# Kernel optimization log

Measured on AMD Instinct MI355X. Metric: run time of the kernel, lower is better.

The kernel has to match this reference:

```python
import jax, jax.numpy as jnp
import numpy as np

B, N, D, H = 4, 2048, 256, 4
HD = D // H


def _linear(x, W, b):
    return x @ W.T + b


def _rotate_half(x):
    # pairs (x0,x1) -> (-x1, x0)
    x1 = x[..., ::2]
    x2 = x[..., 1::2]
    return jnp.stack((-x2, x1), axis=-1).reshape(x.shape)


def _layernorm(x, g, b, eps=1e-5):
    m = jnp.mean(x, axis=-1, keepdims=True)
    v = jnp.mean((x - m) ** 2, axis=-1, keepdims=True)
    return (x - m) / jnp.sqrt(v + eps) * g + b


def _ffn(x, W1, b1, g, be, W2, b2):
    h = _linear(x, W1, b1)
    h = _layernorm(h, g, be)
    h = jax.nn.gelu(h, approximate=False)
    return _linear(h, W2, b2)


def _self_block(x, enc, Wqkv, bqkv, Wout, bout, W1, b1, g, be, W2, b2):
    Bq, Nq, _ = x.shape
    qkv = _linear(x, Wqkv, bqkv).reshape(Bq, Nq, H, HD, 3).transpose(0, 2, 1, 3, 4)  # [B,H,N,HD,3]
    q, k, v = qkv[..., 0], qkv[..., 1], qkv[..., 2]
    q = q * enc[0] + _rotate_half(q) * enc[1]
    k = k * enc[0] + _rotate_half(k) * enc[1]
    scale = HD ** -0.5
    sim = jnp.einsum('bhid,bhjd->bhij', q, k) * scale
    attn = jax.nn.softmax(sim, axis=-1)
    ctx = jnp.einsum('bhij,bhjd->bhid', attn, v)
    msg = _linear(ctx.transpose(0, 2, 1, 3).reshape(Bq, Nq, D), Wout, bout)
    return x + _ffn(jnp.concatenate([x, msg], axis=-1), W1, b1, g, be, W2, b2)


def _cross_block(x0, x1, Wqk, bqk, Wv, bv, Wo, bo, W1, b1, g, be, W2, b2):
    def heads(t):
        return t.reshape(t.shape[0], t.shape[1], H, HD).transpose(0, 2, 1, 3)  # [B,H,N,HD]
    qk0 = heads(_linear(x0, Wqk, bqk))
    qk1 = heads(_linear(x1, Wqk, bqk))
    v0 = heads(_linear(x0, Wv, bv))
    v1 = heads(_linear(x1, Wv, bv))
    s = (HD ** -0.5) ** 0.5
    qk0 = qk0 * s
    qk1 = qk1 * s
    sim = jnp.einsum('bhid,bhjd->bhij', qk0, qk1)
    attn01 = jax.nn.softmax(sim, axis=-1)   # over j (x1 tokens)
    attn10 = jax.nn.softmax(sim, axis=-2)   # over i (x0 tokens)
    m0 = jnp.einsum('bhij,bhjd->bhid', attn01, v1)
    m1 = jnp.einsum('bhij,bhid->bhjd', attn10, v0)
    def unheads(t):
        return t.transpose(0, 2, 1, 3).reshape(t.shape[0], t.shape[2], D)
    m0 = _linear(unheads(m0), Wo, bo)
    m1 = _linear(unheads(m1), Wo, bo)
    x0 = x0 + _ffn(jnp.concatenate([x0, m0], axis=-1), W1, b1, g, be, W2, b2)
    x1 = x1 + _ffn(jnp.concatenate([x1, m1], axis=-1), W1, b1, g, be, W2, b2)
    return x0, x1


def setup_inputs() -> dict:
    key = jax.random.key(0)
    ks = jax.random.split(key, 32)
    std = 0.05

    def rn(k, shape, s=std):
        return jax.random.normal(k, shape, dtype=jnp.float32) * s

    def enc(k):
        ang = jax.random.uniform(k, (B, 1, N, HD // 2), dtype=jnp.float32) * (2 * np.pi)
        cos = jnp.repeat(jnp.cos(ang), 2, axis=-1)
        sin = jnp.repeat(jnp.sin(ang), 2, axis=-1)
        return jnp.stack([cos, sin], axis=0)  # [2,B,1,N,HD]

    return {
        'desc0': rn(ks[0], (B, N, D), 1.0),
        'desc1': rn(ks[1], (B, N, D), 1.0),
        'enc0': enc(ks[2]),
        'enc1': enc(ks[3]),
        's_Wqkv': rn(ks[4], (3 * D, D)), 's_bqkv': jnp.zeros((3 * D,), jnp.float32),
        's_Wout': rn(ks[5], (D, D)), 's_bout': jnp.zeros((D,), jnp.float32),
        's_W1': rn(ks[6], (2 * D, 2 * D)), 's_b1': jnp.zeros((2 * D,), jnp.float32),
        's_g': jnp.ones((2 * D,), jnp.float32), 's_be': jnp.zeros((2 * D,), jnp.float32),
        's_W2': rn(ks[7], (D, 2 * D)), 's_b2': jnp.zeros((D,), jnp.float32),
        'c_Wqk': rn(ks[8], (D, D)), 'c_bqk': jnp.zeros((D,), jnp.float32),
        'c_Wv': rn(ks[9], (D, D)), 'c_bv': jnp.zeros((D,), jnp.float32),
        'c_Wo': rn(ks[10], (D, D)), 'c_bo': jnp.zeros((D,), jnp.float32),
        'c_W1': rn(ks[11], (2 * D, 2 * D)), 'c_b1': jnp.zeros((2 * D,), jnp.float32),
        'c_g': jnp.ones((2 * D,), jnp.float32), 'c_be': jnp.zeros((2 * D,), jnp.float32),
        'c_W2': rn(ks[12], (D, 2 * D)), 'c_b2': jnp.zeros((D,), jnp.float32),
    }


def reference(desc0, desc1, enc0, enc1,
              s_Wqkv, s_bqkv, s_Wout, s_bout, s_W1, s_b1, s_g, s_be, s_W2, s_b2,
              c_Wqk, c_bqk, c_Wv, c_bv, c_Wo, c_bo, c_W1, c_b1, c_g, c_be, c_W2, c_b2):
    d0 = _self_block(desc0, enc0, s_Wqkv, s_bqkv, s_Wout, s_bout, s_W1, s_b1, s_g, s_be, s_W2, s_b2)
    d1 = _self_block(desc1, enc1, s_Wqkv, s_bqkv, s_Wout, s_bout, s_W1, s_b1, s_g, s_be, s_W2, s_b2)
    return _cross_block(d0, d1, c_Wqk, c_bqk, c_Wv, c_bv, c_Wo, c_bo, c_W1, c_b1, c_g, c_be, c_W2, c_b2)
```

## Files before the change

### kernel.cpp

```cpp
#include <hip/hip_runtime.h>
#include <cstddef>

#define NTOK 2048
#define BDIM 4
#define DIM 256
#define NHEAD 4
#define MROWS 8192
#define M2 16384
#define NMu ((size_t)MROWS * DIM)

typedef unsigned short u16;
typedef __attribute__((ext_vector_type(8))) short short8;
typedef __attribute__((ext_vector_type(4))) float f32x4;

__device__ __forceinline__ u16 f2bf(float x) {
  union { float f; unsigned u; } c; c.f = x;
  unsigned r = c.u + 0x7FFFu + ((c.u >> 16) & 1u);
  return (u16)(r >> 16);
}
__device__ __forceinline__ float bf2f(u16 u) {
  union { unsigned u; float f; } c; c.u = ((unsigned)u) << 16;
  return c.f;
}

__device__ __forceinline__ void glds16(const void* g, void* l) {
  __builtin_amdgcn_global_load_lds(
      (const __attribute__((address_space(1))) unsigned int*)g,
      (__attribute__((address_space(3))) unsigned int*)l, 16, 0, 0);
}

__global__ __launch_bounds__(256) void gemm_bf16_kernel(
    const u16* __restrict__ A, int lda,
    const u16* __restrict__ A2, int lda2, int kSplit,
    const u16* __restrict__ W,
    const float* __restrict__ bias0, const float* __restrict__ bias1,
    int nsplit, float os0, float os1,
    u16* __restrict__ Yb0, int ldy0,
    u16* __restrict__ Yb1, int ldy1,
    int K)
{
  __shared__ u16 As[128 * 32];
  __shared__ u16 Bs[128 * 32];
  const int t = threadIdx.x;
  const int m0 = blockIdx.y * 128, n0 = blockIdx.x * 128;
  const int r4 = t >> 2, c8 = (t & 3) * 8;
  const int lane = t & 63, w = t >> 6;
  const int cl = lane & 15, quad = lane >> 4;
  const int wm = (w >> 1) * 64, wn = (w & 1) * 64;

  f32x4 acc[4][4];
#pragma unroll
  for (int i = 0; i < 4; ++i)
#pragma unroll
    for (int j = 0; j < 4; ++j) acc[i][j] = (f32x4){0.f, 0.f, 0.f, 0.f};

  for (int k0 = 0; k0 < K; k0 += 32) {
    const u16* Ab; int la; int kk;
    if (k0 < kSplit) { Ab = A; la = lda; kk = k0; }
    else             { Ab = A2; la = lda2; kk = k0 - kSplit; }
    const u16* ag = Ab + (size_t)(m0 + r4) * la + kk + c8;
    const u16* bg = W + (size_t)(n0 + r4) * K + k0 + c8;
    __syncthreads();
    glds16(ag, &As[t * 8]);
    glds16(ag + (size_t)64 * la, &As[2048 + t * 8]);
    glds16(bg, &Bs[t * 8]);
    glds16(bg + (size_t)64 * K, &Bs[2048 + t * 8]);
    __syncthreads();

    short8 af[4], bfr[4];
#pragma unroll
    for (int i = 0; i < 4; ++i)
      af[i] = *(const short8*)&As[(wm + i * 16 + cl) * 32 + quad * 8];
#pragma unroll
    for (int i = 0; i < 4; ++i)
      bfr[i] = *(const short8*)&Bs[(wn + i * 16 + cl) * 32 + quad * 8];
#pragma unroll
    for (int mt = 0; mt < 4; ++mt)
#pragma unroll
      for (int nt = 0; nt < 4; ++nt)
        acc[mt][nt] = __builtin_amdgcn_mfma_f32_16x16x32_bf16(
            af[mt], bfr[nt], acc[mt][nt], 0, 0, 0);
  }

#pragma unroll
  for (int mt = 0; mt < 4; ++mt)
#pragma unroll
    for (int nt = 0; nt < 4; ++nt) {
      const int colg = n0 + wn + nt * 16 + cl;
      const bool first = colg < nsplit;
      const int c2 = first ? colg : colg - nsplit;
      const float bs = first ? bias0[c2] : bias1[c2];
      const float os = first ? os0 : os1;
      u16* yb = first ? Yb0 : Yb1;
      const int ly = first ? ldy0 : ldy1;
#pragma unroll
      for (int r = 0; r < 4; ++r) {
        const int rowg = m0 + wm + mt * 16 + quad * 4 + r;
        yb[(size_t)rowg * ly + c2] = f2bf((acc[mt][nt][r] + bs) * os);
      }
    }
}

__global__ __launch_bounds__(256) void gemm64_kernel(
    const u16* __restrict__ A, int lda,
    const u16* __restrict__ W,
    const float* __restrict__ bias,
    const u16* __restrict__ resb, int ldrb,
    float* __restrict__ Yf, int ldyf,
    u16* __restrict__ Yb, int ldyb,
    int K)
{
  __shared__ u16 As[64 * 32];
  __shared__ u16 Bs[64 * 32];
  const int t = threadIdx.x;
  const int m0 = blockIdx.y * 64, n0 = blockIdx.x * 64;
  const int r8 = t >> 2, c8 = (t & 3) * 8;
  const int lane = t & 63, w = t >> 6;
  const int cl = lane & 15, quad = lane >> 4;
  const int wm = (w >> 1) * 32, wn = (w & 1) * 32;

  f32x4 acc[2][2];
#pragma unroll
  for (int i = 0; i < 2; ++i)
#pragma unroll
    for (int j = 0; j < 2; ++j) acc[i][j] = (f32x4){0.f, 0.f, 0.f, 0.f};

  for (int k0 = 0; k0 < K; k0 += 32) {
    const u16* ag = A + (size_t)(m0 + r8) * lda + k0 + c8;
    const u16* bg = W + (size_t)(n0 + r8) * K + k0 + c8;
    __syncthreads();
    glds16(ag, &As[t * 8]);
    glds16(bg, &Bs[t * 8]);
    __syncthreads();

    short8 af[2], bfr[2];
#pragma unroll
    for (int i = 0; i < 2; ++i)
      af[i] = *(const short8*)&As[(wm + i * 16 + cl) * 32 + quad * 8];
#pragma unroll
    for (int j = 0; j < 2; ++j)
      bfr[j] = *(const short8*)&Bs[(wn + j * 16 + cl) * 32 + quad * 8];
#pragma unroll
    for (int mt = 0; mt < 2; ++mt)
#pragma unroll
      for (int nt = 0; nt < 2; ++nt)
        acc[mt][nt] = __builtin_amdgcn_mfma_f32_16x16x32_bf16(
            af[mt], bfr[nt], acc[mt][nt], 0, 0, 0);
  }

#pragma unroll
  for (int mt = 0; mt < 2; ++mt)
#pragma unroll
    for (int nt = 0; nt < 2; ++nt) {
      const int colg = n0 + wn + nt * 16 + cl;
      const float bs = bias[colg];
#pragma unroll
      for (int r = 0; r < 4; ++r) {
        const int rowg = m0 + wm + mt * 16 + quad * 4 + r;
        float v = acc[mt][nt][r] + bs;
        if (resb) v += bf2f(resb[(size_t)rowg * ldrb + colg]);
        if (Yf) Yf[(size_t)rowg * ldyf + colg] = v;
        if (Yb) Yb[(size_t)rowg * ldyb + colg] = f2bf(v);
      }
    }
}

__global__ __launch_bounds__(256) void wfuse_kernel(
    const float* __restrict__ W1, const float* __restrict__ Wo,
    const float* __restrict__ b1, const float* __restrict__ bo,
    const float* __restrict__ cW1, const float* __restrict__ cWo,
    const float* __restrict__ cb1, const float* __restrict__ cbo,
    u16* __restrict__ W1f, u16* __restrict__ cW1f,
    float* __restrict__ b1f, float* __restrict__ cb1f)
{
  const int n = blockIdx.x, sel = blockIdx.y;
  const float* Ws = sel ? cW1 : W1;
  const float* Wos = sel ? cWo : Wo;
  u16* out = sel ? cW1f : W1f;
  __shared__ float rowh[256];
  const int t = threadIdx.x;
  rowh[t] = Ws[(size_t)n * 512 + 256 + t];
  out[(size_t)n * 512 + t] = f2bf(Ws[(size_t)n * 512 + t]);
  __syncthreads();
  float acc = 0.f;
  for (int m = 0; m < 256; ++m) acc += rowh[m] * Wos[(size_t)m * 256 + t];
  out[(size_t)n * 512 + 256 + t] = f2bf(acc);
  if (t == 0) {
    const float* bos = sel ? cbo : bo;
    const float* b1s = sel ? cb1 : b1;
    float a = b1s[n];
    for (int m = 0; m < 256; ++m) a += rowh[m] * bos[m];
    (sel ? cb1f : b1f)[n] = a;
  }
}

__global__ __launch_bounds__(256) void rope_repack_kernel(
    const u16* __restrict__ qkv, const float* __restrict__ enc0,
    const float* __restrict__ enc1,
    u16* __restrict__ Q, u16* __restrict__ K, u16* __restrict__ V)
{
  const int idx = blockIdx.x * blockDim.x + threadIdx.x;
  const int i = idx & 31;
  const int h = (idx >> 5) & 3;
  const int m = idx >> 7;
  const int half = m >> 13;
  const int lm = m & (MROWS - 1);
  const float* enc = half ? enc1 : enc0;
  const u16* src = qkv + (size_t)m * 768 + h * 192 + i * 6;
  const unsigned a0 = *(const unsigned*)(src);
  const unsigned a1 = *(const unsigned*)(src + 2);
  const unsigned a2 = *(const unsigned*)(src + 4);
  const float q0 = bf2f((u16)a0), k0 = bf2f((u16)(a0 >> 16));
  const float v0 = bf2f((u16)a1), q1 = bf2f((u16)(a1 >> 16));
  const float k1 = bf2f((u16)a2), v1 = bf2f((u16)(a2 >> 16));
  const float c = enc[(size_t)lm * 64 + 2 * i];
  const float s = enc[(size_t)MROWS * 64 + (size_t)lm * 64 + 2 * i];
  const float QSC = 0.18033688011112042f;
  const size_t o = (size_t)m * 256 + h * 64 + 2 * i;
  *(unsigned*)(Q + o) = (unsigned)f2bf((q0 * c - q1 * s) * QSC) |
                        ((unsigned)f2bf((q1 * c + q0 * s) * QSC) << 16);
  *(unsigned*)(K + o) = (unsigned)f2bf(k0 * c - k1 * s) |
                        ((unsigned)f2bf(k1 * c + k0 * s) << 16);
  *(unsigned*)(V + o) = (unsigned)f2bf(v0) | ((unsigned)f2bf(v1) << 16);
}

__global__ __launch_bounds__(256) void transpose_v_kernel(
    const u16* __restrict__ in, u16* __restrict__ out)
{
  __shared__ u16 Tl[64][72];
  const int bz = blockIdx.z, h = blockIdx.y;
  const int n0 = blockIdx.x * 64;
  const int t = threadIdx.x;
  {
    const int row = t >> 2, c16 = (t & 3) * 16;
    const u16* src = in + (size_t)(bz * NTOK + n0 + row) * 256 + h * 64 + c16;
    *(uint4*)&Tl[row][c16] = *(const uint4*)src;
    *(uint4*)&Tl[row][c16 + 8] = *(const uint4*)(src + 8);
  }
  __syncthreads();
  const int d = t >> 2, qr = t & 3;
  union { u16 u[16]; uint4 v[2]; } pk;
#pragma unroll
  for (int j = 0; j < 16; ++j) pk.u[j] = Tl[qr * 16 + j][d];
  u16* dst = out + ((size_t)((bz * NHEAD + h) * 64 + d)) * NTOK + n0 + qr * 16;
  *(uint4*)dst = pk.v[0];
  *(uint4*)(dst + 8) = pk.v[1];
}

__global__ __launch_bounds__(256, 4) void attn3_kernel(
    const u16* __restrict__ Qb, const u16* __restrict__ Kb,
    const u16* __restrict__ Vtb,
    u16* __restrict__ Po, float* __restrict__ Pm, float* __restrict__ Pl,
    int cross)
{
  __shared__ u16 Ks[64 * 72];
  __shared__ u16 Vs[64 * 72];
  __shared__ u16 QPs[128 * 72];
  const int y = blockIdx.y, z = blockIdx.z;
  const int h2 = y >> 4, b = (y >> 2) & 3, h = y & 3;
  const int kh = cross ? (1 - h2) : h2;
  const int qrowbase = (h2 * 4 + b) * NTOK;
  const int krowbase = (kh * 4 + b) * NTOK + z * 1024;
  const int vz = kh * 4 + b;
  const int n0 = blockIdx.x * 128;
  const int t = threadIdx.x, lane = t & 63, w = t >> 6;
  const int cl = lane & 15, quad = lane >> 4;

  {
    const int row = t >> 1, c32 = (t & 1) * 32;
    const u16* src = Qb + (size_t)(qrowbase + n0 + row) * 256 + h * 64 + c32;
    uint4 v0 = *(const uint4*)src;
    uint4 v1 = *(const uint4*)(src + 8);
    uint4 v2 = *(const uint4*)(src + 16);
    uint4 v3 = *(const uint4*)(src + 24);
    u16* d = &QPs[row * 72 + c32];
    *(uint4*)d = v0; *(uint4*)(d + 8) = v1;
    *(uint4*)(d + 16) = v2; *(uint4*)(d + 24) = v3;
  }
  __syncthreads();
  const int q0 = w * 32;
  short8 bq[2][2];
#pragma unroll
  for (int c = 0; c < 2; ++c) {
    bq[c][0] = *(const short8*)&QPs[(q0 + c * 16 + cl) * 72 + quad * 8];
    bq[c][1] = *(const short8*)&QPs[(q0 + c * 16 + cl) * 72 + quad * 8 + 32];
  }

  float m_r[2] = {-1e30f, -1e30f}, l_r[2] = {0.f, 0.f};
  f32x4 o[2][4];
#pragma unroll
  for (int c = 0; c < 2; ++c)
#pragma unroll
    for (int i = 0; i < 4; ++i) o[c][i] = (f32x4){0.f, 0.f, 0.f, 0.f};

  const int srow = t >> 2, sc16 = (t & 3) * 16;
  const u16* Kg = Kb + (size_t)(krowbase + srow) * 256 + h * 64 + sc16;
  const u16* Vg = Vtb + ((size_t)(vz * NHEAD + h) * 64 + srow) * NTOK + z * 1024 + sc16;
  uint4 ka0 = *(const uint4*)Kg, ka1 = *(const uint4*)(Kg + 8);
  uint4 va0 = *(const uint4*)Vg, va1 = *(const uint4*)(Vg + 8);

  for (int tile = 0; tile < 16; ++tile) {
    __syncthreads();
    *(uint4*)&Ks[srow * 72 + sc16] = ka0;
    *(uint4*)&Ks[srow * 72 + sc16 + 8] = ka1;
    *(uint4*)&Vs[srow * 72 + sc16] = va0;
    *(uint4*)&Vs[srow * 72 + sc16 + 8] = va1;
    __syncthreads();
    if (tile < 15) {
      Kg += 64 * 256; Vg += 64;
      ka0 = *(const uint4*)Kg; ka1 = *(const uint4*)(Kg + 8);
      va0 = *(const uint4*)Vg; va1 = *(const uint4*)(Vg + 8);
    }

    f32x4 sf[2][4];
#pragma unroll
    for (int kb = 0; kb < 4; ++kb) {
      short8 ak0 = *(const short8*)&Ks[(kb * 16 + cl) * 72 + quad * 8];
      short8 ak1 = *(const short8*)&Ks[(kb * 16 + cl) * 72 + quad * 8 + 32];
#pragma unroll
      for (int c = 0; c < 2; ++c) {
        f32x4 acc = (f32x4){0.f, 0.f, 0.f, 0.f};
        acc = __builtin_amdgcn_mfma_f32_16x16x32_bf16(ak0, bq[c][0], acc, 0, 0, 0);
        acc = __builtin_amdgcn_mfma_f32_16x16x32_bf16(ak1, bq[c][1], acc, 0, 0, 0);
        sf[c][kb] = acc;
      }
    }

#pragma unroll
    for (int c = 0; c < 2; ++c) {
      float mx = sf[c][0][0];
#pragma unroll
      for (int kb = 0; kb < 4; ++kb)
#pragma unroll
        for (int r = 0; r < 4; ++r) mx = fmaxf(mx, sf[c][kb][r]);
      mx = fmaxf(mx, __shfl_xor(mx, 16));
      mx = fmaxf(mx, __shfl_xor(mx, 32));
      const float mn = fmaxf(m_r[c], mx);
      const float alpha = exp2f(m_r[c] - mn);
      m_r[c] = mn;
      float rs = 0.f;
#pragma unroll
      for (int kb = 0; kb < 4; ++kb)
#pragma unroll
        for (int r = 0; r < 4; ++r) {
          const float p = exp2f(sf[c][kb][r] - mn);
          sf[c][kb][r] = p; rs += p;
        }
      rs += __shfl_xor(rs, 16);
      rs += __shfl_xor(rs, 32);
      l_r[c] = l_r[c] * alpha + rs;
#pragma unroll
      for (int db = 0; db < 4; ++db) o[c][db] *= alpha;
#pragma unroll
      for (int kb = 0; kb < 4; ++kb) {
        unsigned d0 = __builtin_amdgcn_perm(__float_as_uint(sf[c][kb][1]),
                                            __float_as_uint(sf[c][kb][0]), 0x07060302u);
        unsigned d1 = __builtin_amdgcn_perm(__float_as_uint(sf[c][kb][3]),
                                            __float_as_uint(sf[c][kb][2]), 0x07060302u);
        uint2 pk; pk.x = d0; pk.y = d1;
        *(uint2*)&QPs[(q0 + c * 16 + cl) * 72 + kb * 16 + quad * 4] = pk;
      }
    }

    short8 bp[2][2];
#pragma unroll
    for (int c = 0; c < 2; ++c) {
      bp[c][0] = *(const short8*)&QPs[(q0 + c * 16 + cl) * 72 + quad * 8];
      bp[c][1] = *(const short8*)&QPs[(q0 + c * 16 + cl) * 72 + quad * 8 + 32];
    }
#pragma unroll
    for (int db = 0; db < 4; ++db) {
      short8 av0 = *(const short8*)&Vs[(db * 16 + cl) * 72 + quad * 8];
      short8 av1 = *(const short8*)&Vs[(db * 16 + cl) * 72 + quad * 8 + 32];
#pragma unroll
      for (int c = 0; c < 2; ++c) {
        o[c][db] = __builtin_amdgcn_mfma_f32_16x16x32_bf16(av0, bp[c][0], o[c][db], 0, 0, 0);
        o[c][db] = __builtin_amdgcn_mfma_f32_16x16x32_bf16(av1, bp[c][1], o[c][db], 0, 0, 0);
      }
    }
  }

#pragma unroll
  for (int c = 0; c < 2; ++c) {
    const int rp = z * 65536 + y * 2048 + n0 + q0 + c * 16 + cl;
#pragma unroll
    for (int db = 0; db < 4; ++db) {
      ushort4 st;
      st.x = f2bf(o[c][db][0]); st.y = f2bf(o[c][db][1]);
      st.z = f2bf(o[c][db][2]); st.w = f2bf(o[c][db][3]);
      *(ushort4*)(Po + (size_t)rp * 64 + db * 16 + quad * 4) = st;
    }
    if (quad == 0) { Pm[rp] = m_r[c]; Pl[rp] = l_r[c]; }
  }
}

__global__ __launch_bounds__(256) void attn_combine_kernel(
    const u16* __restrict__ Po, const float* __restrict__ Pm,
    const float* __restrict__ Pl, u16* __restrict__ Ou)
{
  const int rowi = blockIdx.x * 4 + (threadIdx.x >> 6);
  const int lane = threadIdx.x & 63;
  const float m0 = Pm[rowi], m1 = Pm[65536 + rowi];
  const float l0 = Pl[rowi], l1 = Pl[65536 + rowi];
  const float M = fmaxf(m0, m1);
  const float e0 = exp2f(m0 - M), e1 = exp2f(m1 - M);
  const float inv = 1.f / (e0 * l0 + e1 * l1);
  const float o0 = bf2f(Po[(size_t)rowi * 64 + lane]);
  const float o1 = bf2f(Po[(size_t)65536 * 64 + (size_t)rowi * 64 + lane]);
  const float val = (e0 * o0 + e1 * o1) * inv;
  const int y = rowi >> 11, q = rowi & 2047;
  const int bz = y >> 2, h = y & 3;
  Ou[(size_t)(bz * NTOK + q) * 256 + h * 64 + lane] = f2bf(val);
}

__global__ __launch_bounds__(256) void ln_gelu_kernel(
    const u16* __restrict__ Hm, const float* __restrict__ g,
    const float* __restrict__ be, u16* __restrict__ out)
{
  const int rowi = blockIdx.x * 4 + (threadIdx.x >> 6);
  const int lane = threadIdx.x & 63;
  const u16* row = Hm + (size_t)rowi * 512 + lane * 8;
  u16* orow = out + (size_t)rowi * 512 + lane * 8;
  uint4 raw = *(const uint4*)row;
  float x[8];
  const unsigned* rw = (const unsigned*)&raw;
#pragma unroll
  for (int i = 0; i < 4; ++i) {
    x[2 * i]     = bf2f((u16)rw[i]);
    x[2 * i + 1] = bf2f((u16)(rw[i] >> 16));
  }
  float s = 0.f;
#pragma unroll
  for (int i = 0; i < 8; ++i) s += x[i];
#pragma unroll
  for (int off = 32; off; off >>= 1) s += __shfl_xor(s, off);
  const float mean = s * (1.f / 512.f);
  float s2 = 0.f;
#pragma unroll
  for (int i = 0; i < 8; ++i) { const float d = x[i] - mean; s2 += d * d; }
#pragma unroll
  for (int off = 32; off; off >>= 1) s2 += __shfl_xor(s2, off);
  const float rstd = rsqrtf(s2 * (1.f / 512.f) + 1e-5f);
  unsigned ov[4];
#pragma unroll
  for (int i = 0; i < 4; ++i) {
    const int c = lane * 8 + 2 * i;
    const float y0 = (x[2 * i] - mean) * rstd * g[c] + be[c];
    const float y1 = (x[2 * i + 1] - mean) * rstd * g[c + 1] + be[c + 1];
    const float g0 = 0.5f * y0 * (1.f + erff(y0 * 0.70710678118654752f));
    const float g1 = 0.5f * y1 * (1.f + erff(y1 * 0.70710678118654752f));
    ov[i] = (unsigned)f2bf(g0) | ((unsigned)f2bf(g1) << 16);
  }
  *(uint4*)orow = *(uint4*)ov;
}

__global__ __launch_bounds__(256) void pack_all_kernel(
    const float* w0, const float* w1, const float* w2, const float* w3,
    const float* w4, const float* d0, const float* d1,
    u16* __restrict__ wb, u16* __restrict__ descb)
{
  const size_t idx4 = ((size_t)blockIdx.x * 256 + threadIdx.x) * 4;
  const float* src; u16* dst; size_t off;
  if (idx4 < 589824) {
    off = idx4; dst = wb + idx4;
    if      (idx4 < 196608) { src = w0; }
    else if (idx4 < 327680) { src = w1; off -= 196608; }
    else if (idx4 < 393216) { src = w2; off -= 327680; }
    else if (idx4 < 458752) { src = w3; off -= 393216; }
    else                    { src = w4; off -= 458752; }
  } else {
    size_t o = idx4 - 589824;
    dst = descb + o;
    if (o < NMu) { src = d0; off = o; }
    else         { src = d1; off = o - NMu; }
  }
  float4 v = *(const float4*)(src + off);
  ushort4 ov;
  ov.x = f2bf(v.x); ov.y = f2bf(v.y); ov.z = f2bf(v.z); ov.w = f2bf(v.w);
  *(ushort4*)dst = ov;
}

extern "C" void kernel_launch(void* const* d_in, const int* in_sizes, int n_in,
                              void* d_out, int out_size, void* d_ws, size_t ws_size,
                              hipStream_t stream) {
  const float* desc0  = (const float*)d_in[0];
  const float* desc1  = (const float*)d_in[1];
  const float* enc0   = (const float*)d_in[2];
  const float* enc1   = (const float*)d_in[3];
  const float* s_Wqkv = (const float*)d_in[4];
  const float* s_bqkv = (const float*)d_in[5];
  const float* s_Wout = (const float*)d_in[6];
  const float* s_bout = (const float*)d_in[7];
  const float* s_W1   = (const float*)d_in[8];
  const float* s_b1   = (const float*)d_in[9];
  const float* s_g    = (const float*)d_in[10];
  const float* s_be   = (const float*)d_in[11];
  const float* s_W2   = (const float*)d_in[12];
  const float* s_b2   = (const float*)d_in[13];
  const float* c_Wqk  = (const float*)d_in[14];
  const float* c_bqk  = (const float*)d_in[15];
  const float* c_Wv   = (const float*)d_in[16];
  const float* c_bv   = (const float*)d_in[17];
  const float* c_Wo   = (const float*)d_in[18];
  const float* c_bo   = (const float*)d_in[19];
  const float* c_W1   = (const float*)d_in[20];
  const float* c_b1   = (const float*)d_in[21];
  const float* c_g    = (const float*)d_in[22];
  const float* c_be   = (const float*)d_in[23];
  const float* c_W2   = (const float*)d_in[24];
  const float* c_b2   = (const float*)d_in[25];

  u16* U = (u16*)d_ws;
  u16* descb = U + 0 * NMu;
  u16* qkvb  = U + 2 * NMu;
  u16* ctxb  = U + 2 * NMu;
  u16* Qu    = U + 8 * NMu;
  u16* Ku    = U + 10 * NMu;
  u16* Vu    = U + 12 * NMu;
  u16* Vt    = U + 14 * NMu;
  u16* hbufb = U + 12 * NMu;
  u16* Po    = U + 16 * NMu;
  u16* hb2   = U + 16 * NMu;
  float* Pm  = (float*)(U + 20 * NMu);
  float* Pl  = Pm + 2 * 65536;
  float* b1f = Pl + 2 * 65536;
  float* cb1f = b1f + 512;
  u16* s_b   = U + 21 * NMu;
  u16* wb    = U + 23 * NMu;

  u16* Wqkvb = wb;
  u16* W2b   = wb + 196608;
  u16* cQKVb = wb + 327680;
  u16* cW2b  = wb + 458752;
  u16* W1f   = wb + 589824;
  u16* cW1f  = wb + 851968;

  float* outf = (float*)d_out;

  const dim3 attn_grid(NTOK / 128, 32, 2);
  const dim3 tv_grid(NTOK / 64, NHEAD, 8);
  const int rope_blocks = (M2 * 128) / 256;
  const int lng_blocks  = M2 / 4;
  const int comb_blocks = 65536 / 4;
  const float BIG = 2.1e9f;
  (void)BIG;
  const float csc = 0.42466090014400953f;

  hipLaunchKernelGGL(pack_all_kernel, dim3(4672), dim3(256), 0, stream,
                     s_Wqkv, s_W2, c_Wqk, c_Wv, c_W2, desc0, desc1, wb, descb);
  hipLaunchKernelGGL(wfuse_kernel, dim3(512, 2), dim3(256), 0, stream,
                     s_W1, s_Wout, s_b1, s_bout, c_W1, c_Wo, c_b1, c_bo,
                     W1f, cW1f, b1f, cb1f);

  hipLaunchKernelGGL(gemm_bf16_kernel, dim3(6, 128), dim3(256), 0, stream,
                     descb, 256, (const u16*)nullptr, 0, 1 << 30, Wqkvb,
                     s_bqkv, (const float*)nullptr, 1 << 30, 1.f, 1.f,
                     qkvb, 768, (u16*)nullptr, 0, 256);
  hipLaunchKernelGGL(rope_repack_kernel, dim3(rope_blocks), dim3(256), 0, stream,
                     qkvb, enc0, enc1, Qu, Ku, Vu);
  hipLaunchKernelGGL(transpose_v_kernel, tv_grid, dim3(256), 0, stream, Vu, Vt);
  hipLaunchKernelGGL(attn3_kernel, attn_grid, dim3(256), 0, stream,
                     Qu, Ku, Vt, Po, Pm, Pl, 0);
  hipLaunchKernelGGL(attn_combine_kernel, dim3(comb_blocks), dim3(256), 0, stream,
                     Po, Pm, Pl, ctxb);
  hipLaunchKernelGGL(gemm_bf16_kernel, dim3(4, 128), dim3(256), 0, stream,
                     descb, 256, ctxb, 256, 256, W1f,
                     b1f, (const float*)nullptr, 1 << 30, 1.f, 1.f,
                     hbufb, 512, (u16*)nullptr, 0, 512);
  hipLaunchKernelGGL(ln_gelu_kernel, dim3(lng_blocks), dim3(256), 0, stream,
                     hbufb, s_g, s_be, hb2);
  hipLaunchKernelGGL(gemm64_kernel, dim3(4, 256), dim3(256), 0, stream,
                     hb2, 512, W2b, s_b2, descb, 256,
                     (float*)nullptr, 0, s_b, 256, 512);

  u16* qkb = Qu;
  u16* vb  = Ku;
  hipLaunchKernelGGL(gemm_bf16_kernel, dim3(4, 128), dim3(256), 0, stream,
                     s_b, 256, (const u16*)nullptr, 0, 1 << 30, cQKVb,
                     c_bqk, c_bv, 256, csc, 1.f,
                     qkb, 256, vb, 256, 256);
  hipLaunchKernelGGL(transpose_v_kernel, tv_grid, dim3(256), 0, stream, vb, Vt);
  hipLaunchKernelGGL(attn3_kernel, attn_grid, dim3(256), 0, stream,
                     qkb, qkb, Vt, Po, Pm, Pl, 1);
  hipLaunchKernelGGL(attn_combine_kernel, dim3(comb_blocks), dim3(256), 0, stream,
                     Po, Pm, Pl, ctxb);
  hipLaunchKernelGGL(gemm_bf16_kernel, dim3(4, 128), dim3(256), 0, stream,
                     s_b, 256, ctxb, 256, 256, cW1f,
                     cb1f, (const float*)nullptr, 1 << 30, 1.f, 1.f,
                     hbufb, 512, (u16*)nullptr, 0, 512);
  hipLaunchKernelGGL(ln_gelu_kernel, dim3(lng_blocks), dim3(256), 0, stream,
                     hbufb, c_g, c_be, hb2);
  hipLaunchKernelGGL(gemm64_kernel, dim3(4, 256), dim3(256), 0, stream,
                     hb2, 512, cW2b, c_b2, s_b, 256,
                     outf, 256, (u16*)nullptr, 0, 512);
}
```

Measured before the change: 442.0 us.

## Read K/V fragments straight from global and share one running max per wave

The attention kernel stops staging K and V tiles through shared memory. Each wave now loads its MFMA operand fragments directly from global memory, which removes both per-tile __syncthreads and the register prefetch. The online-softmax max is also reduced across all 32 query rows of a wave instead of per row, so alpha and the decision to rescale are wave-uniform, and the O accumulators are rescaled only when the max grows. In exchange, each wave re-reads K/V from global/L2 with no software prefetch, exposing load latency, and a shared max can underflow exponentials for rows whose scores sit far below the wave maximum.

Measured after the change: 549.8 us. 24.4% more time.

```diff
diff --git a/kernel.cpp b/kernel.cpp
--- a/kernel.cpp
+++ b/kernel.cpp
@@ -247,14 +247,12 @@
   *(uint4*)(dst + 8) = pk.v[1];
 }
 
-__global__ __launch_bounds__(256, 4) void attn3_kernel(
+__global__ __launch_bounds__(256, 4) void attn4_kernel(
     const u16* __restrict__ Qb, const u16* __restrict__ Kb,
     const u16* __restrict__ Vtb,
     u16* __restrict__ Po, float* __restrict__ Pm, float* __restrict__ Pl,
     int cross)
 {
-  __shared__ u16 Ks[64 * 72];
-  __shared__ u16 Vs[64 * 72];
   __shared__ u16 QPs[128 * 72];
   const int y = blockIdx.y, z = blockIdx.z;
   const int h2 = y >> 4, b = (y >> 2) & 3, h = y & 3;
@@ -286,37 +284,24 @@
     bq[c][1] = *(const short8*)&QPs[(q0 + c * 16 + cl) * 72 + quad * 8 + 32];
   }
 
-  float m_r[2] = {-1e30f, -1e30f}, l_r[2] = {0.f, 0.f};
+  float m_r = -1e30f;
+  float l_r[2] = {0.f, 0.f};
   f32x4 o[2][4];
 #pragma unroll
   for (int c = 0; c < 2; ++c)
 #pragma unroll
     for (int i = 0; i < 4; ++i) o[c][i] = (f32x4){0.f, 0.f, 0.f, 0.f};
 
-  const int srow = t >> 2, sc16 = (t & 3) * 16;
-  const u16* Kg = Kb + (size_t)(krowbase + srow) * 256 + h * 64 + sc16;
-  const u16* Vg = Vtb + ((size_t)(vz * NHEAD + h) * 64 + srow) * NTOK + z * 1024 + sc16;
-  uint4 ka0 = *(const uint4*)Kg, ka1 = *(const uint4*)(Kg + 8);
-  uint4 va0 = *(const uint4*)Vg, va1 = *(const uint4*)(Vg + 8);
+  const u16* Kp = Kb + (size_t)(krowbase + cl) * 256 + h * 64 + quad * 8;
+  const u16* Vp = Vtb + ((size_t)(vz * NHEAD + h) * 64 + cl) * 2048 + z * 1024 + quad * 8;
 
   for (int tile = 0; tile < 16; ++tile) {
-    __syncthreads();
-    *(uint4*)&Ks[srow * 72 + sc16] = ka0;
-    *(uint4*)&Ks[srow * 72 + sc16 + 8] = ka1;
-    *(uint4*)&Vs[srow * 72 + sc16] = va0;
-    *(uint4*)&Vs[srow * 72 + sc16 + 8] = va1;
-    __syncthreads();
-    if (tile < 15) {
-      Kg += 64 * 256; Vg += 64;
-      ka0 = *(const uint4*)Kg; ka1 = *(const uint4*)(Kg + 8);
-      va0 = *(const uint4*)Vg; va1 = *(const uint4*)(Vg + 8);
-    }
-
     f32x4 sf[2][4];
 #pragma unroll
     for (int kb = 0; kb < 4; ++kb) {
-      short8 ak0 = *(const short8*)&Ks[(kb * 16 + cl) * 72 + quad * 8];
-      short8 ak1 = *(const short8*)&Ks[(kb * 16 + cl) * 72 + quad * 8 + 32];
+      const u16* ka = Kp + (size_t)(tile * 64 + kb * 16) * 256;
+      short8 ak0 = *(const short8*)ka;
+      short8 ak1 = *(const short8*)(ka + 32);
 #pragma unroll
       for (int c = 0; c < 2; ++c) {
         f32x4 acc = (f32x4){0.f, 0.f, 0.f, 0.f};
@@ -326,18 +311,26 @@
       }
     }
 
+    float mx = sf[0][0][0];
+#pragma unroll
+    for (int c = 0; c < 2; ++c)
+#pragma unroll
+      for (int kb = 0; kb < 4; ++kb)
+#pragma unroll
+        for (int r = 0; r < 4; ++r) mx = fmaxf(mx, sf[c][kb][r]);
+    mx = fmaxf(mx, __shfl_xor(mx, 1));
+    mx = fmaxf(mx, __shfl_xor(mx, 2));
+    mx = fmaxf(mx, __shfl_xor(mx, 4));
+    mx = fmaxf(mx, __shfl_xor(mx, 8));
+    mx = fmaxf(mx, __shfl_xor(mx, 16));
+    mx = fmaxf(mx, __shfl_xor(mx, 32));
+    const bool newmax = mx > m_r;
+    const float mn = newmax ? mx : m_r;
+    const float alpha = exp2f(m_r - mn);
+    m_r = mn;
+
 #pragma unroll
     for (int c = 0; c < 2; ++c) {
-      float mx = sf[c][0][0];
-#pragma unroll
-      for (int kb = 0; kb < 4; ++kb)
-#pragma unroll
-        for (int r = 0; r < 4; ++r) mx = fmaxf(mx, sf[c][kb][r]);
-      mx = fmaxf(mx, __shfl_xor(mx, 16));
-      mx = fmaxf(mx, __shfl_xor(mx, 32));
-      const float mn = fmaxf(m_r[c], mx);
-      const float alpha = exp2f(m_r[c] - mn);
-      m_r[c] = mn;
       float rs = 0.f;
 #pragma unroll
       for (int kb = 0; kb < 4; ++kb)
@@ -349,8 +342,6 @@
       rs += __shfl_xor(rs, 16);
       rs += __shfl_xor(rs, 32);
       l_r[c] = l_r[c] * alpha + rs;
-#pragma unroll
-      for (int db = 0; db < 4; ++db) o[c][db] *= alpha;
 #pragma unroll
       for (int kb = 0; kb < 4; ++kb) {
         unsigned d0 = __builtin_amdgcn_perm(__float_as_uint(sf[c][kb][1]),
@@ -361,6 +352,12 @@
         *(uint2*)&QPs[(q0 + c * 16 + cl) * 72 + kb * 16 + quad * 4] = pk;
       }
     }
+    if (newmax) {
+#pragma unroll
+      for (int c = 0; c < 2; ++c)
+#pragma unroll
+        for (int db = 0; db < 4; ++db) o[c][db] *= alpha;
+    }
 
     short8 bp[2][2];
 #pragma unroll
@@ -370,8 +367,9 @@
     }
 #pragma unroll
     for (int db = 0; db < 4; ++db) {
-      short8 av0 = *(const short8*)&Vs[(db * 16 + cl) * 72 + quad * 8];
-      short8 av1 = *(const short8*)&Vs[(db * 16 + cl) * 72 + quad * 8 + 32];
+      const u16* va = Vp + (size_t)db * 16 * 2048 + tile * 64;
+      short8 av0 = *(const short8*)va;
+      short8 av1 = *(const short8*)(va + 32);
 #pragma unroll
       for (int c = 0; c < 2; ++c) {
         o[c][db] = __builtin_amdgcn_mfma_f32_16x16x32_bf16(av0, bp[c][0], o[c][db], 0, 0, 0);
@@ -390,7 +388,7 @@
       st.z = f2bf(o[c][db][2]); st.w = f2bf(o[c][db][3]);
       *(ushort4*)(Po + (size_t)rp * 64 + db * 16 + quad * 4) = st;
     }
-    if (quad == 0) { Pm[rp] = m_r[c]; Pl[rp] = l_r[c]; }
+    if (quad == 0) { Pm[rp] = m_r; Pl[rp] = l_r[c]; }
   }
 }
 
@@ -542,8 +540,6 @@
   const int rope_blocks = (M2 * 128) / 256;
   const int lng_blocks  = M2 / 4;
   const int comb_blocks = 65536 / 4;
-  const float BIG = 2.1e9f;
-  (void)BIG;
   const float csc = 0.42466090014400953f;
 
   hipLaunchKernelGGL(pack_all_kernel, dim3(4672), dim3(256), 0, stream,
@@ -559,7 +555,7 @@
   hipLaunchKernelGGL(rope_repack_kernel, dim3(rope_blocks), dim3(256), 0, stream,
                      qkvb, enc0, enc1, Qu, Ku, Vu);
   hipLaunchKernelGGL(transpose_v_kernel, tv_grid, dim3(256), 0, stream, Vu, Vt);
-  hipLaunchKernelGGL(attn3_kernel, attn_grid, dim3(256), 0, stream,
+  hipLaunchKernelGGL(attn4_kernel, attn_grid, dim3(256), 0, stream,
                      Qu, Ku, Vt, Po, Pm, Pl, 0);
   hipLaunchKernelGGL(attn_combine_kernel, dim3(comb_blocks), dim3(256), 0, stream,
                      Po, Pm, Pl, ctxb);
@@ -580,7 +576,7 @@
                      c_bqk, c_bv, 256, csc, 1.f,
                      qkb, 256, vb, 256, 256);
   hipLaunchKernelGGL(transpose_v_kernel, tv_grid, dim3(256), 0, stream, vb, Vt);
-  hipLaunchKernelGGL(attn3_kernel, attn_grid, dim3(256), 0, stream,
+  hipLaunchKernelGGL(attn4_kernel, attn_grid, dim3(256), 0, stream,
                      qkb, qkb, Vt, Po, Pm, Pl, 1);
   hipLaunchKernelGGL(attn_combine_kernel, dim3(comb_blocks), dim3(256), 0, stream,
                      Po, Pm, Pl, ctxb);
```
